# Kernel optimization log

Hardware: AMD Instinct MI355X
Metric: run time of the kernel (lower is better)

## Reference

```python
import jax, jax.numpy as jnp
import numpy as np

HIDDEN = 1024


def setup_inputs() -> dict:
    key = jax.random.key(0)
    ks = jax.random.split(key, 9)
    B, S, Kq, H = 16, 4096, 64, HIDDEN
    scale = 1.0 / np.sqrt(H)
    return {
        "queries": jax.random.normal(ks[0], (B, Kq, H), jnp.float32),
        "keys": jax.random.normal(ks[1], (B, S, H), jnp.float32),
        "values": jax.random.normal(ks[2], (B, S, H), jnp.float32),
        "Wq": jax.random.normal(ks[3], (H, H), jnp.float32) * scale,
        "bq": jax.random.normal(ks[4], (H,), jnp.float32) * 0.02,
        "Wk": jax.random.normal(ks[5], (H, H), jnp.float32) * scale,
        "bk": jax.random.normal(ks[6], (H,), jnp.float32) * 0.02,
        "Wv": jax.random.normal(ks[7], (H, H), jnp.float32) * scale,
        "bv": jax.random.normal(ks[8], (H,), jnp.float32) * 0.02,
    }


def reference(queries, keys, values, Wq, bq, Wk, bk, Wv, bv):
    H = Wq.shape[0]
    scaling = jax.lax.rsqrt(jnp.asarray(H, queries.dtype))
    # torch Linear: x @ W^T + b
    q = queries @ Wq.T + bq            # (B, Kq, H)
    k = keys @ Wk.T + bk               # (B, S, H)
    v = values @ Wv.T + bv             # (B, S, H)
    # scores: k @ q^T -> (B, S, Kq), softmax over seq_len axis (dim=1)
    scores = jnp.einsum('bsh,bqh->bsq', k, q) * scaling
    attention_weights = jax.nn.softmax(scores, axis=1)
    # context: attn^T @ v -> (B, Kq, H)
    context = jnp.einsum('bsq,bsh->bqh', attention_weights, v)
    return context, attention_weights
```

## Files before the change

### kernel.cpp

```cpp
#include <hip/hip_runtime.h>
#include <hip/hip_bf16.h>

#define H 1024
#define SEQ 4096
#define BQ 64
#define NB 16

typedef float f32x4 __attribute__((ext_vector_type(4)));
typedef __bf16 bf16x8 __attribute__((ext_vector_type(8)));

__device__ __forceinline__ void split_bf16(const float* x, bf16x8& hi, bf16x8& lo)
{
    #pragma unroll
    for (int i = 0; i < 8; ++i) {
        float v = x[i];
        __bf16 h = (__bf16)v;
        hi[i] = h;
        lo[i] = (__bf16)(v - (float)h);
    }
}

__device__ __forceinline__ void gload_lds16(const float* g, void* lds)
{
    __builtin_amdgcn_global_load_lds(
        (const __attribute__((address_space(1))) void*)g,
        (__attribute__((address_space(3))) void*)lds, 16, 0, 0);
}

__global__ __launch_bounds__(256)
void mfma_gemm_bt(const float* __restrict__ A, const float* __restrict__ Bm,
                  const float* __restrict__ bias, float* __restrict__ C, float scale)
{
    const int m0 = blockIdx.x * 64;
    const int n0 = blockIdx.y * 64;
    const int w   = threadIdx.x >> 6;
    const int l   = threadIdx.x & 63;
    const int row = l & 15;
    const int kg  = l >> 4;

    const float* ap = A + (size_t)(m0 + w * 16 + row) * H + kg * 8;
    const float* bp = Bm + (size_t)(n0 + row) * H + kg * 8;

    f32x4 acc[4] = {};
    for (int k0 = 0; k0 < H; k0 += 32) {
        float a8[8];
        *reinterpret_cast<float4*>(&a8[0]) = *reinterpret_cast<const float4*>(ap + k0);
        *reinterpret_cast<float4*>(&a8[4]) = *reinterpret_cast<const float4*>(ap + k0 + 4);
        bf16x8 ahi, alo;
        split_bf16(a8, ahi, alo);
        #pragma unroll
        for (int j = 0; j < 4; ++j) {
            float b8[8];
            const float* bjp = bp + (size_t)j * 16 * H + k0;
            *reinterpret_cast<float4*>(&b8[0]) = *reinterpret_cast<const float4*>(bjp);
            *reinterpret_cast<float4*>(&b8[4]) = *reinterpret_cast<const float4*>(bjp + 4);
            bf16x8 bhi, blo;
            split_bf16(b8, bhi, blo);
            acc[j] = __builtin_amdgcn_mfma_f32_16x16x32_bf16(ahi, bhi, acc[j], 0, 0, 0);
            acc[j] = __builtin_amdgcn_mfma_f32_16x16x32_bf16(ahi, blo, acc[j], 0, 0, 0);
            acc[j] = __builtin_amdgcn_mfma_f32_16x16x32_bf16(alo, bhi, acc[j], 0, 0, 0);
        }
    }
    #pragma unroll
    for (int j = 0; j < 4; ++j) {
        int n = n0 + j * 16 + row;
        float bb = bias ? bias[n] : 0.f;
        #pragma unroll
        for (int r = 0; r < 4; ++r) {
            int m = m0 + w * 16 + kg * 4 + r;
            C[(size_t)m * H + n] = acc[j][r] * scale + bb;
        }
    }
}

__global__ __launch_bounds__(256)
void transpose_k(const float* __restrict__ Wk, float* __restrict__ WkT)
{
    __shared__ float tile[64][65];
    const int k0 = blockIdx.x * 64;
    const int n0 = blockIdx.y * 64;
    const int t  = threadIdx.x;
    const int c4 = (t & 15) * 4;
    const int r  = t >> 4;
    #pragma unroll
    for (int p = 0; p < 4; ++p) {
        float4 v = *reinterpret_cast<const float4*>(&Wk[(size_t)(k0 + r + 16 * p) * H + n0 + c4]);
        tile[r + 16 * p][c4 + 0] = v.x;
        tile[r + 16 * p][c4 + 1] = v.y;
        tile[r + 16 * p][c4 + 2] = v.z;
        tile[r + 16 * p][c4 + 3] = v.w;
    }
    __syncthreads();
    #pragma unroll
    for (int p = 0; p < 4; ++p) {
        int rr = r + 16 * p;
        float4 o;
        o.x = tile[c4 + 0][rr];
        o.y = tile[c4 + 1][rr];
        o.z = tile[c4 + 2][rr];
        o.w = tile[c4 + 3][rr];
        *reinterpret_cast<float4*>(&WkT[(size_t)(n0 + rr) * H + k0 + c4]) = o;
    }
}

__global__ __launch_bounds__(256)
void ngemm_bt(const float* __restrict__ A, const float* __restrict__ Bm,
              __bf16* __restrict__ Nhi, __bf16* __restrict__ Nlo, float scale)
{
    const int m0 = blockIdx.x * 64;
    const int n0 = blockIdx.y * 64;
    const int w   = threadIdx.x >> 6;
    const int l   = threadIdx.x & 63;
    const int row = l & 15;
    const int kg  = l >> 4;

    const float* ap = A + (size_t)(m0 + w * 16 + row) * H + kg * 8;
    const float* bp = Bm + (size_t)(n0 + row) * H + kg * 8;

    f32x4 acc[4] = {};
    for (int k0 = 0; k0 < H; k0 += 32) {
        float a8[8];
        *reinterpret_cast<float4*>(&a8[0]) = *reinterpret_cast<const float4*>(ap + k0);
        *reinterpret_cast<float4*>(&a8[4]) = *reinterpret_cast<const float4*>(ap + k0 + 4);
        bf16x8 ahi, alo;
        split_bf16(a8, ahi, alo);
        #pragma unroll
        for (int j = 0; j < 4; ++j) {
            float b8[8];
            const float* bjp = bp + (size_t)j * 16 * H + k0;
            *reinterpret_cast<float4*>(&b8[0]) = *reinterpret_cast<const float4*>(bjp);
            *reinterpret_cast<float4*>(&b8[4]) = *reinterpret_cast<const float4*>(bjp + 4);
            bf16x8 bhi, blo;
            split_bf16(b8, bhi, blo);
            acc[j] = __builtin_amdgcn_mfma_f32_16x16x32_bf16(ahi, bhi, acc[j], 0, 0, 0);
            acc[j] = __builtin_amdgcn_mfma_f32_16x16x32_bf16(ahi, blo, acc[j], 0, 0, 0);
            acc[j] = __builtin_amdgcn_mfma_f32_16x16x32_bf16(alo, bhi, acc[j], 0, 0, 0);
        }
    }
    #pragma unroll
    for (int j = 0; j < 4; ++j) {
        int n = n0 + j * 16 + row;
        #pragma unroll
        for (int r = 0; r < 4; ++r) {
            int m = m0 + w * 16 + kg * 4 + r;
            float v = acc[j][r] * scale;
            __bf16 hi = (__bf16)v;
            Nhi[(size_t)m * H + n] = hi;
            Nlo[(size_t)m * H + n] = (__bf16)(v - (float)hi);
        }
    }
}

__global__ __launch_bounds__(256)
void cvec_kernel(const float* __restrict__ q, const float* __restrict__ bk,
                 float* __restrict__ cvec, float scale)
{
    int r = blockIdx.x * 4 + (threadIdx.x >> 6);
    int l = threadIdx.x & 63;
    float s = 0.f;
    #pragma unroll
    for (int i = 0; i < 16; ++i)
        s += q[(size_t)r * H + l + 64 * i] * bk[l + 64 * i];
    #pragma unroll
    for (int off = 32; off; off >>= 1)
        s += __shfl_down(s, off);
    if (l == 0) cvec[r] = s * scale;
}

__global__ __launch_bounds__(512)
void scores_mfma(const float* __restrict__ keys,
                 const __bf16* __restrict__ Nhi, const __bf16* __restrict__ Nlo,
                 const float* __restrict__ cvec, float* __restrict__ scores)
{
    const int id = blockIdx.x;
    const int x  = id & 7;
    const int m  = id >> 3;
    const int b  = 2 * x + (m >> 5);
    const int s0 = (m & 31) * 128;

    const int t   = threadIdx.x;
    const int w   = t >> 6;
    const int l   = t & 63;
    const int row = l & 15;
    const int kg  = l >> 4;

    __shared__ __bf16 nshH[64][16][8];
    __shared__ __bf16 nshL[64][16][8];

    const float* ka = keys + ((size_t)b * SEQ + s0 + w * 16 + row) * H + kg * 8;
    const __bf16* nhb = Nhi + (size_t)b * BQ * H;
    const __bf16* nlb = Nlo + (size_t)b * BQ * H;

    const int sqi = (t >> 4) & 31;
    const int skb = t & 15;
    const int ssl = skb ^ (sqi & 7);

    f32x4 acc[4] = {};
    for (int c = 0; c < 8; ++c) {
        const int kc = c * 128;
        float4 kr[8];
        #pragma unroll
        for (int ii = 0; ii < 4; ++ii) {
            kr[2 * ii + 0] = *reinterpret_cast<const float4*>(ka + kc + ii * 32);
            kr[2 * ii + 1] = *reinterpret_cast<const float4*>(ka + kc + ii * 32 + 4);
        }
        bf16x8 nh[2], nl[2];
        #pragma unroll
        for (int rep = 0; rep < 2; ++rep) {
            size_t go = (size_t)(rep * 32 + sqi) * H + kc + skb * 8;
            nh[rep] = *reinterpret_cast<const bf16x8*>(nhb + go);
            nl[rep] = *reinterpret_cast<const bf16x8*>(nlb + go);
        }
        __syncthreads();
        #pragma unroll
        for (int rep = 0; rep < 2; ++rep) {
            *reinterpret_cast<bf16x8*>(&nshH[rep * 32 + sqi][ssl][0]) = nh[rep];
            *reinterpret_cast<bf16x8*>(&nshL[rep * 32 + sqi][ssl][0]) = nl[rep];
        }
        __syncthreads();
        #pragma unroll
        for (int ii = 0; ii < 4; ++ii) {
            float a8[8];
            *reinterpret_cast<float4*>(&a8[0]) = kr[2 * ii + 0];
            *reinterpret_cast<float4*>(&a8[4]) = kr[2 * ii + 1];
            bf16x8 ahi, alo;
            split_bf16(a8, ahi, alo);
            const int kb = ii * 4 + kg;
            const int slot = kb ^ (row & 7);
            #pragma unroll
            for (int j = 0; j < 4; ++j) {
                const int qi = j * 16 + row;
                bf16x8 bhi = *reinterpret_cast<const bf16x8*>(&nshH[qi][slot][0]);
                bf16x8 blo = *reinterpret_cast<const bf16x8*>(&nshL[qi][slot][0]);
                acc[j] = __builtin_amdgcn_mfma_f32_16x16x32_bf16(ahi, bhi, acc[j], 0, 0, 0);
                acc[j] = __builtin_amdgcn_mfma_f32_16x16x32_bf16(ahi, blo, acc[j], 0, 0, 0);
                acc[j] = __builtin_amdgcn_mfma_f32_16x16x32_bf16(alo, bhi, acc[j], 0, 0, 0);
            }
        }
    }
    #pragma unroll
    for (int j = 0; j < 4; ++j) {
        int qi = j * 16 + row;
        float cv = cvec[b * BQ + qi];
        #pragma unroll
        for (int r = 0; r < 4; ++r) {
            int s = s0 + w * 16 + kg * 4 + r;
            scores[((size_t)b * SEQ + s) * BQ + qi] = acc[j][r] + cv;
        }
    }
}

__global__ __launch_bounds__(256)
void sm_partial(const float* __restrict__ scores, float* __restrict__ pmax,
                float* __restrict__ psum)
{
    const int b  = blockIdx.y;
    const int ch = blockIdx.x;
    const int t  = threadIdx.x;
    const int qi = t & 63;
    const int g  = t >> 6;
    const float* sb = scores + ((size_t)b * SEQ + ch * 128) * BQ;
    float v[32];
    #pragma unroll
    for (int i = 0; i < 32; ++i)
        v[i] = sb[(size_t)(g + i * 4) * BQ + qi];
    float m = v[0];
    #pragma unroll
    for (int i = 1; i < 32; ++i) m = fmaxf(m, v[i]);
    __shared__ float red[4][64];
    red[g][qi] = m;
    __syncthreads();
    float M = fmaxf(fmaxf(red[0][qi], red[1][qi]), fmaxf(red[2][qi], red[3][qi]));
    float sum = 0.f;
    #pragma unroll
    for (int i = 0; i < 32; ++i) sum += __expf(v[i] - M);
    __syncthreads();
    red[g][qi] = sum;
    __syncthreads();
    if (g == 0) {
        float ssum = red[0][qi] + red[1][qi] + red[2][qi] + red[3][qi];
        pmax[((size_t)b * 32 + ch) * 64 + qi] = M;
        psum[((size_t)b * 32 + ch) * 64 + qi] = ssum;
    }
}

__global__ void sm_combine(const float* __restrict__ pmax,
                           const float* __restrict__ psum,
                           float* __restrict__ gstat)
{
    int b  = blockIdx.x;
    int qi = threadIdx.x;
    float m = -1e30f;
    for (int c = 0; c < 32; ++c)
        m = fmaxf(m, pmax[((size_t)b * 32 + c) * 64 + qi]);
    float s = 0.f;
    for (int c = 0; c < 32; ++c)
        s += psum[((size_t)b * 32 + c) * 64 + qi] *
             __expf(pmax[((size_t)b * 32 + c) * 64 + qi] - m);
    gstat[(size_t)b * 64 + qi] = m;
    gstat[(size_t)(NB + b) * 64 + qi] = 1.f / s;
}

__global__ __launch_bounds__(256)
void sm_norm(float* __restrict__ attn, const float* __restrict__ gstat,
             __hip_bfloat16* __restrict__ abfT)
{
    __shared__ float tile[64][133];
    const int b  = blockIdx.y;
    const int ch = blockIdx.x;
    const int t  = threadIdx.x;
    const int qi = t & 63;
    const int g  = t >> 6;
    const float M   = gstat[(size_t)b * 64 + qi];
    const float inv = gstat[(size_t)(NB + b) * 64 + qi];
    float* sb = attn + ((size_t)b * SEQ + ch * 128) * BQ;
    #pragma unroll 8
    for (int i = 0; i < 32; ++i) {
        int sl = g + i * 4;
        size_t idx = (size_t)sl * BQ + qi;
        float w = __expf(sb[idx] - M) * inv;
        sb[idx] = w;
        tile[qi][sl] = w;
    }
    __syncthreads();
    const int qo = t >> 2;
    const int c  = (t & 3) * 32;
    __hip_bfloat16* dst = abfT + ((size_t)(b * BQ + qo)) * SEQ + ch * 128 + c;
    #pragma unroll
    for (int v = 0; v < 4; ++v) {
        bf16x8 w8;
        #pragma unroll
        for (int e = 0; e < 8; ++e)
            w8[e] = (__bf16)tile[qo][c + v * 8 + e];
        *reinterpret_cast<bf16x8*>(dst + v * 8) = w8;
    }
}

template<int SC>
__global__ __launch_bounds__(256)
void tmat_mfma(const __hip_bfloat16* __restrict__ abfT,
               const float* __restrict__ values,
               float* __restrict__ Tpart)
{
    const int i  = blockIdx.x;
    const int h0 = ((i >> 3) & 7) * 128;
    const int g  = (i & 7) + 8 * (i >> 6);
    const int b  = g / SC;
    const int sc = g % SC;
    const int schunk = SEQ / SC;

    const int w   = threadIdx.x >> 6;
    const int l   = threadIdx.x & 63;
    const int row = l & 15;
    const int kg  = l >> 4;
    const int sbase = sc * schunk;

    __shared__ float vlds[2][32][128];

    const __hip_bfloat16* ap = abfT + ((size_t)b * BQ + row) * SEQ + sbase + kg * 8;
    const float* vb = values + ((size_t)b * SEQ + sbase) * H + h0;

    const int nk = schunk / 32;

    #define STAGE(buf, k0)                                                     \
        {                                                                      \
            _Pragma("unroll")                                                  \
            for (int ii = 0; ii < 4; ++ii) {                                   \
                int elem = w * 1024 + ii * 256 + l * 4;                        \
                int k    = elem >> 7;                                          \
                int cc   = elem & 127;                                         \
                int csw  = cc ^ ((k >> 3) << 4);                               \
                const float* src = vb + (size_t)((k0) + k) * H + csw;          \
                gload_lds16(src, (void*)(&vlds[buf][0][0] + w * 1024 + ii * 256)); \
            }                                                                  \
        }

    f32x4 acc[4][2] = {};
    STAGE(0, 0);
    __syncthreads();

    for (int ks = 0; ks < nk; ++ks) {
        const int buf = ks & 1;
        if (ks + 1 < nk) STAGE(buf ^ 1, (ks + 1) * 32);
        const int k0 = ks * 32;
        bf16x8 a[4];
        #pragma unroll
        for (int q = 0; q < 4; ++q)
            a[q] = *reinterpret_cast<const bf16x8*>(ap + (size_t)q * 16 * SEQ + k0);
        #pragma unroll
        for (int j = 0; j < 2; ++j) {
            const int col = (w * 32 + j * 16 + row) ^ (kg << 4);
            float b8[8];
            #pragma unroll
            for (int e = 0; e < 8; ++e)
                b8[e] = vlds[buf][kg * 8 + e][col];
            bf16x8 bhi, blo;
            split_bf16(b8, bhi, blo);
            #pragma unroll
            for (int q = 0; q < 4; ++q) {
                acc[q][j] = __builtin_amdgcn_mfma_f32_16x16x32_bf16(a[q], bhi, acc[q][j], 0, 0, 0);
                acc[q][j] = __builtin_amdgcn_mfma_f32_16x16x32_bf16(a[q], blo, acc[q][j], 0, 0, 0);
            }
        }
        __syncthreads();
    }
    #undef STAGE

    float* tp = Tpart + ((size_t)sc * NB + b) * BQ * H;
    #pragma unroll
    for (int q = 0; q < 4; ++q) {
        #pragma unroll
        for (int j = 0; j < 2; ++j) {
            int h = h0 + w * 32 + j * 16 + row;
            #pragma unroll
            for (int r = 0; r < 4; ++r) {
                int qi = q * 16 + kg * 4 + r;
                tp[(size_t)qi * H + h] = acc[q][j][r];
            }
        }
    }
}

template<int SC>
__global__ __launch_bounds__(256)
void tsum_kernel(float* __restrict__ Tpart)
{
    const size_t stride = (size_t)NB * BQ * H;
    size_t i = ((size_t)blockIdx.x * 256 + threadIdx.x) * 4;
    f32x4 s = *reinterpret_cast<const f32x4*>(Tpart + i);
    #pragma unroll
    for (int p = 1; p < SC; ++p)
        s += *reinterpret_cast<const f32x4*>(Tpart + p * stride + i);
    *reinterpret_cast<f32x4*>(Tpart + i) = s;
}

extern "C" void kernel_launch(void* const* d_in, const int* in_sizes, int n_in,
                              void* d_out, int out_size, void* d_ws, size_t ws_size,
                              hipStream_t stream)
{
    const float* queries = (const float*)d_in[0];
    const float* keys    = (const float*)d_in[1];
    const float* values  = (const float*)d_in[2];
    const float* Wq = (const float*)d_in[3];
    const float* bq = (const float*)d_in[4];
    const float* Wk = (const float*)d_in[5];
    const float* bk = (const float*)d_in[6];
    const float* Wv = (const float*)d_in[7];
    const float* bv = (const float*)d_in[8];

    float* out     = (float*)d_out;
    float* context = out;
    float* attn    = out + (size_t)NB * BQ * H;

    const int SC = (ws_size >= (41ull << 20)) ? 8 : 2;

    char* ws = (char*)d_ws;
    float* q     = (float*)ws;
    float* WkT   = (float*)(ws + (4ull << 20));
    __bf16* Nhi  = (__bf16*)(ws + (8ull << 20));
    __bf16* Nlo  = (__bf16*)(ws + (10ull << 20));
    float* Tpart = (float*)ws;
    __hip_bfloat16* abfT = (__hip_bfloat16*)(ws + (size_t)SC * (4ull << 20));
    char* smalls = ws + (size_t)SC * (4ull << 20) + (8ull << 20);
    float* cvec  = (float*)smalls;
    float* gstat = (float*)(smalls + (64u << 10));
    float* pmax  = (float*)(smalls + (128u << 10));
    float* psum  = (float*)(smalls + (512u << 10));

    const float scale = 0.03125f;

    transpose_k<<<dim3(16, 16), 256, 0, stream>>>(Wk, WkT);
    mfma_gemm_bt<<<dim3(16, 16), 256, 0, stream>>>(queries, Wq, bq, q, 1.0f);
    ngemm_bt<<<dim3(16, 16), 256, 0, stream>>>(q, WkT, Nhi, Nlo, scale);
    cvec_kernel<<<256, 256, 0, stream>>>(q, bk, cvec, scale);
    scores_mfma<<<512, 512, 0, stream>>>(keys, Nhi, Nlo, cvec, attn);
    sm_partial<<<dim3(32, NB), 256, 0, stream>>>(attn, pmax, psum);
    sm_combine<<<NB, 64, 0, stream>>>(pmax, psum, gstat);
    sm_norm<<<dim3(32, NB), 256, 0, stream>>>(attn, gstat, abfT);
    if (SC == 8) tmat_mfma<8><<<8 * NB * 8, 256, 0, stream>>>(abfT, values, Tpart);
    else         tmat_mfma<2><<<8 * NB * 2, 256, 0, stream>>>(abfT, values, Tpart);
    if (SC == 8) tsum_kernel<8><<<1024, 256, 0, stream>>>(Tpart);
    else         tsum_kernel<2><<<1024, 256, 0, stream>>>(Tpart);
    mfma_gemm_bt<<<dim3(16, 16), 256, 0, stream>>>(Tpart, Wv, bv, context, 1.0f);
}
```

Baseline: 287.2 us.

## Fuse softmax partial stats into scores kernel and split-K small GEMMs

The per-chunk softmax max and sum-of-exponentials are now computed inside the scores kernel from the register accumulators, using shuffles and a small shared reduction. This removes the separate sm_partial kernel, which re-read the whole score matrix. The three 1024x1024 GEMMs are merged into one templated kernel that uses 512 threads, splitting K in half across two wave groups and combining the halves through shared memory. This doubles the waves available to hide latency, at the cost of an extra barrier and shared-memory traffic.

```diff
diff --git a/kernel.cpp b/kernel.cpp
--- a/kernel.cpp
+++ b/kernel.cpp
@@ -27,22 +27,27 @@
         (__attribute__((address_space(3))) void*)lds, 16, 0, 0);
 }
 
-__global__ __launch_bounds__(256)
-void mfma_gemm_bt(const float* __restrict__ A, const float* __restrict__ Bm,
-                  const float* __restrict__ bias, float* __restrict__ C, float scale)
+template<int MODE>
+__global__ __launch_bounds__(512)
+void gemm_bt_512(const float* __restrict__ A, const float* __restrict__ Bm,
+                 const float* __restrict__ bias, float* __restrict__ C,
+                 __bf16* __restrict__ Nhi, __bf16* __restrict__ Nlo, float scale)
 {
     const int m0 = blockIdx.x * 64;
     const int n0 = blockIdx.y * 64;
-    const int w   = threadIdx.x >> 6;
-    const int l   = threadIdx.x & 63;
+    const int t   = threadIdx.x;
+    const int w   = t >> 6;
+    const int wm  = w & 3;
+    const int kh  = w >> 2;
+    const int l   = t & 63;
     const int row = l & 15;
     const int kg  = l >> 4;
 
-    const float* ap = A + (size_t)(m0 + w * 16 + row) * H + kg * 8;
-    const float* bp = Bm + (size_t)(n0 + row) * H + kg * 8;
+    const float* ap = A + (size_t)(m0 + wm * 16 + row) * H + kh * 512 + kg * 8;
+    const float* bp = Bm + (size_t)(n0 + row) * H + kh * 512 + kg * 8;
 
     f32x4 acc[4] = {};
-    for (int k0 = 0; k0 < H; k0 += 32) {
+    for (int k0 = 0; k0 < 512; k0 += 32) {
         float a8[8];
         *reinterpret_cast<float4*>(&a8[0]) = *reinterpret_cast<const float4*>(ap + k0);
         *reinterpret_cast<float4*>(&a8[4]) = *reinterpret_cast<const float4*>(ap + k0 + 4);
@@ -61,14 +66,35 @@
             acc[j] = __builtin_amdgcn_mfma_f32_16x16x32_bf16(alo, bhi, acc[j], 0, 0, 0);
         }
     }
-    #pragma unroll
-    for (int j = 0; j < 4; ++j) {
-        int n = n0 + j * 16 + row;
-        float bb = bias ? bias[n] : 0.f;
-        #pragma unroll
-        for (int r = 0; r < 4; ++r) {
-            int m = m0 + w * 16 + kg * 4 + r;
-            C[(size_t)m * H + n] = acc[j][r] * scale + bb;
+
+    __shared__ f32x4 red[4][4][64];
+    if (kh == 1) {
+        #pragma unroll
+        for (int j = 0; j < 4; ++j) red[wm][j][l] = acc[j];
+    }
+    __syncthreads();
+    if (kh == 0) {
+        #pragma unroll
+        for (int j = 0; j < 4; ++j) {
+            f32x4 s = acc[j] + red[wm][j][l];
+            int n = n0 + j * 16 + row;
+            if (MODE == 0) {
+                float bb = bias ? bias[n] : 0.f;
+                #pragma unroll
+                for (int r = 0; r < 4; ++r) {
+                    int m = m0 + wm * 16 + kg * 4 + r;
+                    C[(size_t)m * H + n] = s[r] * scale + bb;
+                }
+            } else {
+                #pragma unroll
+                for (int r = 0; r < 4; ++r) {
+                    int m = m0 + wm * 16 + kg * 4 + r;
+                    float v = s[r] * scale;
+                    __bf16 hi = (__bf16)v;
+                    Nhi[(size_t)m * H + n] = hi;
+                    Nlo[(size_t)m * H + n] = (__bf16)(v - (float)hi);
+                }
+            }
         }
     }
 }
@@ -104,54 +130,6 @@
 }
 
 __global__ __launch_bounds__(256)
-void ngemm_bt(const float* __restrict__ A, const float* __restrict__ Bm,
-              __bf16* __restrict__ Nhi, __bf16* __restrict__ Nlo, float scale)
-{
-    const int m0 = blockIdx.x * 64;
-    const int n0 = blockIdx.y * 64;
-    const int w   = threadIdx.x >> 6;
-    const int l   = threadIdx.x & 63;
-    const int row = l & 15;
-    const int kg  = l >> 4;
-
-    const float* ap = A + (size_t)(m0 + w * 16 + row) * H + kg * 8;
-    const float* bp = Bm + (size_t)(n0 + row) * H + kg * 8;
-
-    f32x4 acc[4] = {};
-    for (int k0 = 0; k0 < H; k0 += 32) {
-        float a8[8];
-        *reinterpret_cast<float4*>(&a8[0]) = *reinterpret_cast<const float4*>(ap + k0);
-        *reinterpret_cast<float4*>(&a8[4]) = *reinterpret_cast<const float4*>(ap + k0 + 4);
-        bf16x8 ahi, alo;
-        split_bf16(a8, ahi, alo);
-        #pragma unroll
-        for (int j = 0; j < 4; ++j) {
-            float b8[8];
-            const float* bjp = bp + (size_t)j * 16 * H + k0;
-            *reinterpret_cast<float4*>(&b8[0]) = *reinterpret_cast<const float4*>(bjp);
-            *reinterpret_cast<float4*>(&b8[4]) = *reinterpret_cast<const float4*>(bjp + 4);
-            bf16x8 bhi, blo;
-            split_bf16(b8, bhi, blo);
-            acc[j] = __builtin_amdgcn_mfma_f32_16x16x32_bf16(ahi, bhi, acc[j], 0, 0, 0);
-            acc[j] = __builtin_amdgcn_mfma_f32_16x16x32_bf16(ahi, blo, acc[j], 0, 0, 0);
-            acc[j] = __builtin_amdgcn_mfma_f32_16x16x32_bf16(alo, bhi, acc[j], 0, 0, 0);
-        }
-    }
-    #pragma unroll
-    for (int j = 0; j < 4; ++j) {
-        int n = n0 + j * 16 + row;
-        #pragma unroll
-        for (int r = 0; r < 4; ++r) {
-            int m = m0 + w * 16 + kg * 4 + r;
-            float v = acc[j][r] * scale;
-            __bf16 hi = (__bf16)v;
-            Nhi[(size_t)m * H + n] = hi;
-            Nlo[(size_t)m * H + n] = (__bf16)(v - (float)hi);
-        }
-    }
-}
-
-__global__ __launch_bounds__(256)
 void cvec_kernel(const float* __restrict__ q, const float* __restrict__ bk,
                  float* __restrict__ cvec, float scale)
 {
@@ -170,13 +148,15 @@
 __global__ __launch_bounds__(512)
 void scores_mfma(const float* __restrict__ keys,
                  const __bf16* __restrict__ Nhi, const __bf16* __restrict__ Nlo,
-                 const float* __restrict__ cvec, float* __restrict__ scores)
+                 const float* __restrict__ cvec, float* __restrict__ scores,
+                 float* __restrict__ pmax, float* __restrict__ psum)
 {
     const int id = blockIdx.x;
     const int x  = id & 7;
     const int m  = id >> 3;
     const int b  = 2 * x + (m >> 5);
-    const int s0 = (m & 31) * 128;
+    const int ch = m & 31;
+    const int s0 = ch * 128;
 
     const int t   = threadIdx.x;
     const int w   = t >> 6;
@@ -186,6 +166,7 @@
 
     __shared__ __bf16 nshH[64][16][8];
     __shared__ __bf16 nshL[64][16][8];
+    __shared__ float redm[8][64];
 
     const float* ka = keys + ((size_t)b * SEQ + s0 + w * 16 + row) * H + kg * 8;
     const __bf16* nhb = Nhi + (size_t)b * BQ * H;
@@ -238,49 +219,67 @@
             }
         }
     }
+
     #pragma unroll
     for (int j = 0; j < 4; ++j) {
         int qi = j * 16 + row;
         float cv = cvec[b * BQ + qi];
         #pragma unroll
         for (int r = 0; r < 4; ++r) {
+            acc[j][r] += cv;
             int s = s0 + w * 16 + kg * 4 + r;
-            scores[((size_t)b * SEQ + s) * BQ + qi] = acc[j][r] + cv;
-        }
-    }
-}
-
-__global__ __launch_bounds__(256)
-void sm_partial(const float* __restrict__ scores, float* __restrict__ pmax,
-                float* __restrict__ psum)
-{
-    const int b  = blockIdx.y;
-    const int ch = blockIdx.x;
-    const int t  = threadIdx.x;
-    const int qi = t & 63;
-    const int g  = t >> 6;
-    const float* sb = scores + ((size_t)b * SEQ + ch * 128) * BQ;
-    float v[32];
-    #pragma unroll
-    for (int i = 0; i < 32; ++i)
-        v[i] = sb[(size_t)(g + i * 4) * BQ + qi];
-    float m = v[0];
-    #pragma unroll
-    for (int i = 1; i < 32; ++i) m = fmaxf(m, v[i]);
-    __shared__ float red[4][64];
-    red[g][qi] = m;
-    __syncthreads();
-    float M = fmaxf(fmaxf(red[0][qi], red[1][qi]), fmaxf(red[2][qi], red[3][qi]));
-    float sum = 0.f;
-    #pragma unroll
-    for (int i = 0; i < 32; ++i) sum += __expf(v[i] - M);
-    __syncthreads();
-    red[g][qi] = sum;
-    __syncthreads();
-    if (g == 0) {
-        float ssum = red[0][qi] + red[1][qi] + red[2][qi] + red[3][qi];
-        pmax[((size_t)b * 32 + ch) * 64 + qi] = M;
-        psum[((size_t)b * 32 + ch) * 64 + qi] = ssum;
+            scores[((size_t)b * SEQ + s) * BQ + qi] = acc[j][r];
+        }
+    }
+    float mj[4];
+    #pragma unroll
+    for (int j = 0; j < 4; ++j) {
+        float mm = fmaxf(fmaxf(acc[j][0], acc[j][1]), fmaxf(acc[j][2], acc[j][3]));
+        mm = fmaxf(mm, __shfl_xor(mm, 16));
+        mm = fmaxf(mm, __shfl_xor(mm, 32));
+        mj[j] = mm;
+    }
+    __syncthreads();
+    if (kg == 0) {
+        #pragma unroll
+        for (int j = 0; j < 4; ++j) redm[w][j * 16 + row] = mj[j];
+    }
+    __syncthreads();
+    float Mj[4];
+    #pragma unroll
+    for (int j = 0; j < 4; ++j) {
+        const int qi = j * 16 + row;
+        float M = redm[0][qi];
+        #pragma unroll
+        for (int ww = 1; ww < 8; ++ww) M = fmaxf(M, redm[ww][qi]);
+        Mj[j] = M;
+    }
+    float sj[4];
+    #pragma unroll
+    for (int j = 0; j < 4; ++j) {
+        float s = 0.f;
+        #pragma unroll
+        for (int r = 0; r < 4; ++r) s += __expf(acc[j][r] - Mj[j]);
+        s += __shfl_xor(s, 16);
+        s += __shfl_xor(s, 32);
+        sj[j] = s;
+    }
+    __syncthreads();
+    if (kg == 0) {
+        #pragma unroll
+        for (int j = 0; j < 4; ++j) redm[w][j * 16 + row] = sj[j];
+    }
+    __syncthreads();
+    if (w == 0 && kg == 0) {
+        #pragma unroll
+        for (int j = 0; j < 4; ++j) {
+            const int qi = j * 16 + row;
+            float ss = 0.f;
+            #pragma unroll
+            for (int ww = 0; ww < 8; ++ww) ss += redm[ww][qi];
+            pmax[((size_t)b * 32 + ch) * 64 + qi] = Mj[j];
+            psum[((size_t)b * 32 + ch) * 64 + qi] = ss;
+        }
     }
 }
 
@@ -470,16 +469,18 @@
     const float scale = 0.03125f;
 
     transpose_k<<<dim3(16, 16), 256, 0, stream>>>(Wk, WkT);
-    mfma_gemm_bt<<<dim3(16, 16), 256, 0, stream>>>(queries, Wq, bq, q, 1.0f);
-    ngemm_bt<<<dim3(16, 16), 256, 0, stream>>>(q, WkT, Nhi, Nlo, scale);
+    gemm_bt_512<0><<<dim3(16, 16), 512, 0, stream>>>(
+        queries, Wq, bq, q, nullptr, nullptr, 1.0f);
+    gemm_bt_512<1><<<dim3(16, 16), 512, 0, stream>>>(
+        q, WkT, nullptr, nullptr, Nhi, Nlo, scale);
     cvec_kernel<<<256, 256, 0, stream>>>(q, bk, cvec, scale);
-    scores_mfma<<<512, 512, 0, stream>>>(keys, Nhi, Nlo, cvec, attn);
-    sm_partial<<<dim3(32, NB), 256, 0, stream>>>(attn, pmax, psum);
+    scores_mfma<<<512, 512, 0, stream>>>(keys, Nhi, Nlo, cvec, attn, pmax, psum);
     sm_combine<<<NB, 64, 0, stream>>>(pmax, psum, gstat);
     sm_norm<<<dim3(32, NB), 256, 0, stream>>>(attn, gstat, abfT);
     if (SC == 8) tmat_mfma<8><<<8 * NB * 8, 256, 0, stream>>>(abfT, values, Tpart);
     else         tmat_mfma<2><<<8 * NB * 2, 256, 0, stream>>>(abfT, values, Tpart);
     if (SC == 8) tsum_kernel<8><<<1024, 256, 0, stream>>>(Tpart);
     else         tsum_kernel<2><<<1024, 256, 0, stream>>>(Tpart);
-    mfma_gemm_bt<<<dim3(16, 16), 256, 0, stream>>>(Tpart, Wv, bv, context, 1.0f);
-}
+    gemm_bt_512<0><<<dim3(16, 16), 512, 0, stream>>>(
+        Tpart, Wv, bv, context, nullptr, nullptr, 1.0f);
+}
```

New measurement: 284.8 us. Within noise of the previous version (-0.8%).
